# Optimization experiments

Hardware: AMD Instinct MI355X
Metric: run time of the kernel (lower is better)

Reference implementation:

```python
import jax, jax.numpy as jnp
import numpy as np
from jax import lax

DIM, D_STATE, D_CONV, EXPAND = 96, 16, 4, 2
D_INNER = EXPAND * DIM          # 192
DT_RANK = (DIM + 15) // 16      # 6
B_, T_, H_, W_ = 2, 8, 32, 32   # L = T*H*W = 8192 tokens


def setup_inputs() -> dict:
    key = jax.random.key(0)
    ks = jax.random.split(key, 16)
    f = jnp.float32
    rn = lambda k, shape, s=0.02: jax.random.normal(k, shape, dtype=f) * s
    # S4D-real init for A_log, as in mamba_ssm
    A_init = jnp.log(jnp.tile(jnp.arange(1, D_STATE + 1, dtype=f), (D_INNER, 1)))
    return dict(
        x=jax.random.normal(ks[0], (B_, DIM, T_, H_, W_), dtype=f),
        ln_gamma=1.0 + rn(ks[1], (DIM,)),
        ln_beta=rn(ks[2], (DIM,)),
        in_proj_w=rn(ks[3], (2 * D_INNER, DIM)),
        conv_w=rn(ks[4], (D_INNER, 1, D_CONV), 0.1),
        conv_b=rn(ks[5], (D_INNER,)),
        x_proj_w=rn(ks[6], (DT_RANK + 2 * D_STATE, D_INNER)),
        dt_proj_w=rn(ks[7], (D_INNER, DT_RANK), 0.1),
        dt_proj_b=rn(ks[8], (D_INNER,)) + 0.5,
        A_log=A_init,
        D=jnp.ones((D_INNER,), f),
        conv_w_b=rn(ks[9], (D_INNER, 1, D_CONV), 0.1),
        conv_b_b=rn(ks[10], (D_INNER,)),
        x_proj_w_b=rn(ks[11], (DT_RANK + 2 * D_STATE, D_INNER)),
        dt_proj_w_b=rn(ks[12], (D_INNER, DT_RANK), 0.1),
        dt_proj_b_b=rn(ks[13], (D_INNER,)) + 0.5,
        A_log_b=A_init,
        D_b=jnp.ones((D_INNER,), f),
        out_proj_w=rn(ks[14], (DIM, D_INNER)),
    )


def serpentine(x):
    # continues_scan: reverse W on odd H rows so flattened (T,H,W) ordering is a
    # continuous path through the volume. Involutive => also rev_continues_scan.
    return x.at[..., 1::2, :].set(jnp.flip(x[..., 1::2, :], axis=-1))


def layer_norm(x, g, b, eps=1e-5):
    mu = jnp.mean(x, -1, keepdims=True)
    var = jnp.var(x, -1, keepdims=True)
    return (x - mu) * lax.rsqrt(var + eps) * g + b


def mamba_dir(x_in, z, conv_w, conv_b, x_proj_w, dt_proj_w, dt_proj_b, A_log, D):
    # x_in, z: (B, L, d_inner). One directional selective-scan branch.
    xc = lax.conv_general_dilated(
        x_in.swapaxes(1, 2), conv_w, (1,), [(D_CONV - 1, 0)],
        feature_group_count=D_INNER, dimension_numbers=('NCH', 'OIH', 'NCH'))
    xc = jax.nn.silu(xc + conv_b[None, :, None]).swapaxes(1, 2)  # (B,L,d_inner)
    dbl = jnp.einsum('bld,ed->ble', xc, x_proj_w)                # (B,L,dt_rank+2N)
    dt = jax.nn.softplus(
        jnp.einsum('blr,dr->bld', dbl[..., :DT_RANK], dt_proj_w) + dt_proj_b)
    Bm = dbl[..., DT_RANK:DT_RANK + D_STATE]                     # (B,L,N)
    Cm = dbl[..., DT_RANK + D_STATE:]                            # (B,L,N)
    A = -jnp.exp(A_log)                                          # (d_inner,N)

    def step(h, inp):
        dt_t, x_t, B_t, C_t = inp                                # (B,d),(B,d),(B,N),(B,N)
        h = jnp.exp(dt_t[..., None] * A) * h + (dt_t * x_t)[..., None] * B_t[:, None, :]
        return h, jnp.einsum('bdn,bn->bd', h, C_t)

    h0 = jnp.zeros((x_in.shape[0], D_INNER, D_STATE), x_in.dtype)
    xs = (dt.swapaxes(0, 1), xc.swapaxes(0, 1), Bm.swapaxes(0, 1), Cm.swapaxes(0, 1))
    _, ys = lax.scan(step, h0, xs)                               # (L,B,d_inner)
    y = ys.swapaxes(0, 1) + D * xc
    return y * jax.nn.silu(z)


def reference(x, ln_gamma, ln_beta, in_proj_w, conv_w, conv_b, x_proj_w,
              dt_proj_w, dt_proj_b, A_log, D, conv_w_b, conv_b_b, x_proj_w_b,
              dt_proj_w_b, dt_proj_b_b, A_log_b, D_b, out_proj_w):
    B, C, T, H, W = x.shape
    xs = serpentine(x)
    x_flat = xs.reshape(B, C, T * H * W).swapaxes(1, 2)          # (B,L,dim)
    xn = layer_norm(x_flat, ln_gamma, ln_beta)
    xz = jnp.einsum('bld,ed->ble', xn, in_proj_w)                # (B,L,2*d_inner)
    x_in, z = jnp.split(xz, 2, axis=-1)
    y_f = mamba_dir(x_in, z, conv_w, conv_b, x_proj_w, dt_proj_w,
                    dt_proj_b, A_log, D)
    y_b = jnp.flip(
        mamba_dir(jnp.flip(x_in, 1), jnp.flip(z, 1), conv_w_b, conv_b_b,
                  x_proj_w_b, dt_proj_w_b, dt_proj_b_b, A_log_b, D_b), 1)
    out = jnp.einsum('bld,ed->ble', y_f + y_b, out_proj_w)       # (B,L,dim)
    out = out.swapaxes(1, 2).reshape(B, C, T, H, W)
    return serpentine(out)
```

## Files before the change

### kernel.cpp

```cpp
#include <hip/hip_runtime.h>
#include <math.h>

#define LSEQ 8192
#define TS   32
#define NST  8

template<int CTRL>
__device__ __forceinline__ float dpp_add(float x) {
  const int y = __builtin_amdgcn_update_dpp(0, __float_as_int(x), CTRL, 0xF, 0xF, true);
  return x + __int_as_float(y);
}
__device__ __forceinline__ float red8(float x) {
  x = dpp_add<0xB1>(x);
  x = dpp_add<0x4E>(x);
  x += __int_as_float(__builtin_amdgcn_ds_swizzle(__float_as_int(x), 0x101F));
  return x;
}

__global__ __launch_bounds__(256) void k0_wt(const float* __restrict__ xw_f,
    const float* __restrict__ xw_b, const float* __restrict__ in_w,
    const float* __restrict__ ow, float* __restrict__ xwT,
    float* __restrict__ inwT, float* __restrict__ owT) {
  const int step = gridDim.x * 256;
  const int t0 = blockIdx.x * 256 + threadIdx.x;
  for (int idx = t0; idx < 2 * 192 * 40; idx += step) {
    const int dir = idx / (192 * 40), rem = idx - dir * 192 * 40;
    const int k = rem / 40, r = rem - k * 40;
    const float* w = dir ? xw_b : xw_f;
    xwT[idx] = (r < 38) ? w[r * 192 + k] : 0.f;
  }
  for (int idx = t0; idx < 96 * 384; idx += step) {
    const int k = idx / 384, e = idx - k * 384;
    inwT[idx] = in_w[e * 96 + k];
  }
  for (int idx = t0; idx < 192 * 96; idx += step) {
    const int k = idx / 96, e = idx - k * 96;
    owT[idx] = ow[e * 192 + k];
  }
}

__global__ __launch_bounds__(256) void k1_serp_ln(const float* __restrict__ x,
    const float* __restrict__ gam, const float* __restrict__ bet,
    float* __restrict__ xnT) {
  const int b  = blockIdx.x >> 7;
  const int l0 = (blockIdx.x & 127) << 6;
  __shared__ float xs[96][65];
  __shared__ float mu[64], rs[64];
  const int tid = threadIdx.x;
  for (int idx = tid; idx < 96 * 64; idx += 256) {
    const int c = idx >> 6, l = idx & 63;
    const int lg = l0 + l;
    const int hh = (lg >> 5) & 31, w = lg & 31;
    const int lsrc = (hh & 1) ? (lg + 31 - 2 * w) : lg;
    xs[c][l] = x[(b * 96 + c) * LSEQ + lsrc];
  }
  __syncthreads();
  {
    const int l = tid >> 2, k = tid & 3;
    float s = 0.f, s2 = 0.f;
    for (int c = k; c < 96; c += 4) { const float v = xs[c][l]; s += v; s2 += v * v; }
    s  += __shfl_xor(s, 1);  s  += __shfl_xor(s, 2);
    s2 += __shfl_xor(s2, 1); s2 += __shfl_xor(s2, 2);
    if (k == 0) {
      const float m = s * (1.f / 96.f);
      const float var = s2 * (1.f / 96.f) - m * m;
      mu[l] = m; rs[l] = rsqrtf(var + 1e-5f);
    }
  }
  __syncthreads();
  for (int idx = tid; idx < 96 * 64; idx += 256) {
    const int c = idx >> 6, l = idx & 63;
    xnT[c * 16384 + (b << 13) + l0 + l] =
        (xs[c][l] - mu[l]) * rs[l] * gam[c] + bet[c];
  }
}

__global__ __launch_bounds__(256) void k2_inproj(const float* __restrict__ xnT,
    const float* __restrict__ inwT, float* __restrict__ xz) {
  const int m0 = blockIdx.x << 6;
  const int e0 = blockIdx.y << 6;
  __shared__ float As[96][68];
  __shared__ float Ws[96][68];
  const int tid = threadIdx.x;
  for (int idx = tid; idx < 96 * 64; idx += 256) {
    const int k = idx >> 6, r = idx & 63;
    As[k][r] = xnT[(size_t)k * 16384 + m0 + r];
    Ws[k][r] = inwT[k * 384 + e0 + r];
  }
  __syncthreads();
  const int tx = tid & 15, ty = tid >> 4;
  const int la = tx << 2, ea = ty << 2;
  float acc[4][4] = {};
  for (int k = 0; k < 96; ++k) {
    const float4 av = *(const float4*)&As[k][la];
    const float4 bv = *(const float4*)&Ws[k][ea];
    acc[0][0] = fmaf(bv.x, av.x, acc[0][0]); acc[0][1] = fmaf(bv.x, av.y, acc[0][1]);
    acc[0][2] = fmaf(bv.x, av.z, acc[0][2]); acc[0][3] = fmaf(bv.x, av.w, acc[0][3]);
    acc[1][0] = fmaf(bv.y, av.x, acc[1][0]); acc[1][1] = fmaf(bv.y, av.y, acc[1][1]);
    acc[1][2] = fmaf(bv.y, av.z, acc[1][2]); acc[1][3] = fmaf(bv.y, av.w, acc[1][3]);
    acc[2][0] = fmaf(bv.z, av.x, acc[2][0]); acc[2][1] = fmaf(bv.z, av.y, acc[2][1]);
    acc[2][2] = fmaf(bv.z, av.z, acc[2][2]); acc[2][3] = fmaf(bv.z, av.w, acc[2][3]);
    acc[3][0] = fmaf(bv.w, av.x, acc[3][0]); acc[3][1] = fmaf(bv.w, av.y, acc[3][1]);
    acc[3][2] = fmaf(bv.w, av.z, acc[3][2]); acc[3][3] = fmaf(bv.w, av.w, acc[3][3]);
  }
  const int b = m0 >> 13, l0 = m0 & (LSEQ - 1);
  const bool dos = (e0 >= 192);
#pragma unroll
  for (int j = 0; j < 4; ++j) {
    const int e = e0 + ea + j;
    float4 v;
    v.x = acc[j][0]; v.y = acc[j][1]; v.z = acc[j][2]; v.w = acc[j][3];
    if (dos) {
      v.x = v.x / (1.f + __expf(-v.x)); v.y = v.y / (1.f + __expf(-v.y));
      v.z = v.z / (1.f + __expf(-v.z)); v.w = v.w / (1.f + __expf(-v.w));
    }
    *(float4*)(&xz[((size_t)b * 384 + e) * LSEQ + l0 + la]) = v;
  }
}

__global__ __launch_bounds__(256) void k3a_conv(const float* __restrict__ xz,
    const float* __restrict__ cw_f, const float* __restrict__ cb_f,
    const float* __restrict__ cw_b, const float* __restrict__ cb_b,
    float* __restrict__ xc) {
  const int l = (blockIdx.x << 8) + threadIdx.x;
  const int d = blockIdx.y, b = blockIdx.z;
  const float* xin = xz + ((size_t)b * 384 + d) * LSEQ;
  float xv[7];
#pragma unroll
  for (int j = -3; j <= 3; ++j) {
    const int ls = l + j;
    xv[j + 3] = ((unsigned)ls < LSEQ) ? xin[ls] : 0.f;
  }
  float af = cb_f[d], ab = cb_b[d];
#pragma unroll
  for (int j = 0; j < 4; ++j) {
    af = fmaf(cw_f[d * 4 + j], xv[j], af);
    ab = fmaf(cw_b[d * 4 + j], xv[6 - j], ab);
  }
  xc[((size_t)(b)       * 192 + d) * LSEQ + l] = af / (1.f + __expf(-af));
  xc[((size_t)(2 + b)   * 192 + d) * LSEQ + l] = ab / (1.f + __expf(-ab));
}

__global__ __launch_bounds__(256, 2) void k3b_xproj(const float* __restrict__ xc,
    const float* __restrict__ xwT,
    const float* __restrict__ dtw_f, const float* __restrict__ dtb_f,
    const float* __restrict__ dtw_b, const float* __restrict__ dtb_b,
    float* __restrict__ dt, float* __restrict__ Bo, float* __restrict__ Co) {
  __shared__ float xs[96][66];
  __shared__ float part[4][38][65];
  __shared__ float sdbl[6][65];
  const int dirb = blockIdx.y, dir = dirb >> 1;
  const int tid = threadIdx.x;
  const int lane = tid & 63, w = tid >> 6;
  const int l0 = blockIdx.x << 6;
  const float* pcBase = xc + (size_t)dirb * 192 * LSEQ + l0;
  const float* wt = xwT + dir * 192 * 40;
  float acc[38];
#pragma unroll
  for (int r = 0; r < 38; ++r) acc[r] = 0.f;
  const int kb = 24 * w;
  for (int h = 0; h < 2; ++h) {
    __syncthreads();
    for (int idx = tid; idx < 96 * 64; idx += 256) {
      const int kk = idx >> 6, cc = idx & 63;
      xs[kk][cc] = pcBase[(size_t)(96 * h + kk) * LSEQ + cc];
    }
    __syncthreads();
#pragma unroll 4
    for (int kk = 0; kk < 24; ++kk) {
      const int k = 96 * h + kb + kk;
      const float v = xs[kb + kk][lane];
      const float* wk = wt + k * 40;
#pragma unroll
      for (int r = 0; r < 38; ++r) acc[r] = fmaf(wk[r], v, acc[r]);
    }
  }
#pragma unroll
  for (int r = 0; r < 38; ++r) part[w][r][lane] = acc[r];
  __syncthreads();
  {
    const int lq = tid >> 2, g = tid & 3;
    float vB[4], vC[4];
#pragma unroll
    for (int i = 0; i < 4; ++i) {
      const int rB = 6 + 4 * g + i, rC = 22 + 4 * g + i;
      float sB = 0.f, sC = 0.f;
#pragma unroll
      for (int ww = 0; ww < 4; ++ww) {
        sB += part[ww][rB][lq];
        sC += part[ww][rC][lq];
      }
      vB[i] = sB; vC[i] = sC;
    }
    const size_t off = ((size_t)dirb * LSEQ + l0 + lq) * 16 + 4 * g;
    *(float4*)&Bo[off] = make_float4(vB[0], vB[1], vB[2], vB[3]);
    *(float4*)&Co[off] = make_float4(vC[0], vC[1], vC[2], vC[3]);
  }
  for (int r = w; r < 6; r += 4) {
    float s = 0.f;
#pragma unroll
    for (int ww = 0; ww < 4; ++ww) s += part[ww][r][lane];
    sdbl[r][lane] = s;
  }
  __syncthreads();
  const float* dw = dir ? dtw_b : dtw_f;
  const float* db = dir ? dtb_b : dtb_f;
  const float v0 = sdbl[0][lane], v1 = sdbl[1][lane], v2 = sdbl[2][lane],
              v3 = sdbl[3][lane], v4 = sdbl[4][lane], v5 = sdbl[5][lane];
  float* pdt = dt + (size_t)dirb * 192 * LSEQ + l0 + lane;
#pragma unroll 2
  for (int i = 0; i < 48; ++i) {
    const int d = w * 48 + i;
    float s = db[d];
    s = fmaf(dw[d * 6 + 0], v0, s);
    s = fmaf(dw[d * 6 + 1], v1, s);
    s = fmaf(dw[d * 6 + 2], v2, s);
    s = fmaf(dw[d * 6 + 3], v3, s);
    s = fmaf(dw[d * 6 + 4], v4, s);
    s = fmaf(dw[d * 6 + 5], v5, s);
    pdt[(size_t)d * LSEQ] = (s > 20.f) ? s : __logf(1.f + __expf(s));
  }
}

template<int DIR>
__device__ __forceinline__ void scanA_body(
    float2 (*sdt)[32][34], float (*sb)[TS][16],
    const float* __restrict__ dtg, const float* __restrict__ xcg,
    const float* __restrict__ pB, const float* __restrict__ Al,
    float* __restrict__ Pb, float* __restrict__ Hb, int b, int c, int dg) {
  const int tid = threadIdx.x;
  const int dl = tid >> 3, n = tid & 7;
  const int dirb = DIR * 2 + b;
  const int d = (dg << 5) + dl;
  const float Adn1 = -__expf(Al[d * 16 + n]);
  const float Adn2 = -__expf(Al[d * 16 + n + 8]);
  const size_t rowbase = ((size_t)(dirb * 192) + (dg << 5)) * LSEQ;
  const float* dtp = dtg + rowbase;
  const float* xcp = xcg + rowbase;
  const int c0 = c << 8;
  const int sr0 = tid >> 4, spr = (tid & 15) * 2, sr1 = sr0 + 16;
  const int wt = tid >> 2, wf = (tid & 3) * 4;
  {
    const int tc = c0 + (DIR ? (NST - 1) : 0) * TS;
    const float2 a0 = *(const float2*)&dtp[(size_t)sr0 * LSEQ + tc + spr];
    const float2 x0 = *(const float2*)&xcp[(size_t)sr0 * LSEQ + tc + spr];
    const float2 a1 = *(const float2*)&dtp[(size_t)sr1 * LSEQ + tc + spr];
    const float2 x1 = *(const float2*)&xcp[(size_t)sr1 * LSEQ + tc + spr];
    float4 k0; k0.x = a0.x; k0.y = a0.x * x0.x; k0.z = a0.y; k0.w = a0.y * x0.y;
    float4 k1; k1.x = a1.x; k1.y = a1.x * x1.x; k1.z = a1.y; k1.w = a1.y * x1.y;
    *(float4*)&sdt[0][sr0][spr] = k0;
    *(float4*)&sdt[0][sr1][spr] = k1;
    if (tid < 128) {
      const float4 bv = *(const float4*)&pB[(size_t)(tc + wt) * 16 + wf];
      *(float4*)&sb[0][wt][wf] = bv;
    }
  }
  __syncthreads();
  float h1 = 0.f, h2 = 0.f, dts = 0.f;
  int buf = 0;
  for (int i = 0; i < NST; ++i) {
    const int s = DIR ? (NST - 1 - i) : i;
    float2 a0 = make_float2(0.f, 0.f), x0 = a0, a1 = a0, x1 = a0;
    float4 bv = make_float4(0.f, 0.f, 0.f, 0.f);
    if (i + 1 < NST) {
      const int tn = c0 + (DIR ? (s - 1) : (s + 1)) * TS;
      a0 = *(const float2*)&dtp[(size_t)sr0 * LSEQ + tn + spr];
      x0 = *(const float2*)&xcp[(size_t)sr0 * LSEQ + tn + spr];
      a1 = *(const float2*)&dtp[(size_t)sr1 * LSEQ + tn + spr];
      x1 = *(const float2*)&xcp[(size_t)sr1 * LSEQ + tn + spr];
      if (tid < 128) bv = *(const float4*)&pB[(size_t)(tn + wt) * 16 + wf];
    }
#pragma unroll
    for (int tt = 0; tt < TS; ++tt) {
      const int t = DIR ? (TS - 1 - tt) : tt;
      const float2 xv = sdt[buf][dl][t];
      const float B1 = sb[buf][t][n];
      const float B2 = sb[buf][t][n + 8];
      const float e1 = __expf(xv.x * Adn1);
      const float e2 = __expf(xv.x * Adn2);
      h1 = fmaf(e1, h1, xv.y * B1);
      h2 = fmaf(e2, h2, xv.y * B2);
      dts += xv.x;
    }
    if (i + 1 < NST) {
      float4 k0; k0.x = a0.x; k0.y = a0.x * x0.x; k0.z = a0.y; k0.w = a0.y * x0.y;
      float4 k1; k1.x = a1.x; k1.y = a1.x * x1.x; k1.z = a1.y; k1.w = a1.y * x1.y;
      *(float4*)&sdt[buf ^ 1][sr0][spr] = k0;
      *(float4*)&sdt[buf ^ 1][sr1][spr] = k1;
      if (tid < 128) *(float4*)&sb[buf ^ 1][wt][wf] = bv;
    }
    __syncthreads();
    buf ^= 1;
  }
  const int o = ((dirb * 32 + c) * 192 + d) * 16 + n;
  Pb[o]     = __expf(dts * Adn1);
  Pb[o + 8] = __expf(dts * Adn2);
  Hb[o]     = h1;
  Hb[o + 8] = h2;
}

__global__ __launch_bounds__(256) void k4_scanA(const float* __restrict__ dtg,
    const float* __restrict__ xcg, const float* __restrict__ Bo,
    const float* __restrict__ Al_f, const float* __restrict__ Al_b,
    float* __restrict__ Pb, float* __restrict__ Hb) {
  __shared__ float2 sdt[2][32][34];
  __shared__ float sb[2][TS][16];
  const int b = blockIdx.y, c = blockIdx.x & 31, dg = blockIdx.x >> 5;
  const float* pB0 = Bo + (size_t)(0 * 2 + b) * LSEQ * 16;
  const float* pB1 = Bo + (size_t)(1 * 2 + b) * LSEQ * 16;
  if (blockIdx.z == 0) scanA_body<0>(sdt, sb, dtg, xcg, pB0, Al_f, Pb, Hb, b, c, dg);
  else                 scanA_body<1>(sdt, sb, dtg, xcg, pB1, Al_b, Pb, Hb, b, c, dg);
}

__global__ __launch_bounds__(256) void k5_scanB(const float* __restrict__ Pb,
    const float* __restrict__ Hb, float* __restrict__ H0) {
  const int g = blockIdx.x * 256 + threadIdx.x;
  const int dirb = g / 3072, dn = g - dirb * 3072;
  const int dir = dirb >> 1;
  const int base = dirb * (32 * 3072) + dn;
  float h = 0.f;
  if (dir == 0) {
    for (int c = 0; c < 32; ++c) {
      const int o = base + c * 3072;
      H0[o] = h;
      h = fmaf(Pb[o], h, Hb[o]);
    }
  } else {
    for (int c = 31; c >= 0; --c) {
      const int o = base + c * 3072;
      H0[o] = h;
      h = fmaf(Pb[o], h, Hb[o]);
    }
  }
}

template<int DIR>
__device__ __forceinline__ void scanC_body(
    float2 (*sdt)[32][34], float2 (*sbc)[TS][16],
    const float* __restrict__ dtg, const float* __restrict__ xcg,
    const float* __restrict__ pB, const float* __restrict__ pC,
    const float* __restrict__ xz,
    const float* __restrict__ Al, const float* __restrict__ Dv_,
    const float* __restrict__ H0, float* __restrict__ yout,
    int b, int c, int dg) {
  const int tid = threadIdx.x;
  const int dl = tid >> 3, n = tid & 7;
  const int dirb = DIR * 2 + b;
  const int d = (dg << 5) + dl;
  const float Adn1 = -__expf(Al[d * 16 + n]);
  const float Adn2 = -__expf(Al[d * 16 + n + 8]);
  const float Dv = Dv_[d];
  const size_t rowbase = ((size_t)(dirb * 192) + (dg << 5)) * LSEQ;
  const float* dtp = dtg + rowbase;
  const float* xcp = xcg + rowbase;
  const float* xcq = xcg + ((size_t)(dirb * 192) + d) * LSEQ;
  const float* psp = xz + ((size_t)(b * 384) + 192 + d) * LSEQ;
  float* py = yout + ((size_t)(b * 192) + d) * LSEQ;
  const int o = ((dirb * 32 + c) * 192 + d) * 16 + n;
  float h1 = H0[o], h2 = H0[o + 8];
  const int c0 = c << 8;
  const int sr0 = tid >> 4, spr = (tid & 15) * 2, sr1 = sr0 + 16;
  const int sbt = tid >> 3, sbp = (tid & 7) * 2;
  float cx0, cx1, cx2, cx3, sp0, sp1, sp2, sp3;
  {
    const int tc = c0 + (DIR ? (NST - 1) : 0) * TS;
    const float2 a0 = *(const float2*)&dtp[(size_t)sr0 * LSEQ + tc + spr];
    const float2 x0 = *(const float2*)&xcp[(size_t)sr0 * LSEQ + tc + spr];
    const float2 a1 = *(const float2*)&dtp[(size_t)sr1 * LSEQ + tc + spr];
    const float2 x1 = *(const float2*)&xcp[(size_t)sr1 * LSEQ + tc + spr];
    const float2 b2 = *(const float2*)&pB[(size_t)(tc + sbt) * 16 + sbp];
    const float2 c2 = *(const float2*)&pC[(size_t)(tc + sbt) * 16 + sbp];
    float4 k0; k0.x = a0.x; k0.y = a0.x * x0.x; k0.z = a0.y; k0.w = a0.y * x0.y;
    float4 k1; k1.x = a1.x; k1.y = a1.x * x1.x; k1.z = a1.y; k1.w = a1.y * x1.y;
    *(float4*)&sdt[0][sr0][spr] = k0;
    *(float4*)&sdt[0][sr1][spr] = k1;
    *(float4*)&sbc[0][sbt][sbp] = make_float4(b2.x, c2.x, b2.y, c2.y);
    cx0 = xcq[tc + n];      cx1 = xcq[tc + 8 + n];
    cx2 = xcq[tc + 16 + n]; cx3 = xcq[tc + 24 + n];
    sp0 = psp[tc + n];      sp1 = psp[tc + 8 + n];
    sp2 = psp[tc + 16 + n]; sp3 = psp[tc + 24 + n];
  }
  __syncthreads();
  int buf = 0;
  for (int i = 0; i < NST; ++i) {
    const int s = DIR ? (NST - 1 - i) : i;
    const int t0 = c0 + s * TS;
    float2 a0 = make_float2(0.f, 0.f), x0 = a0, a1 = a0, x1 = a0, b2 = a0, c2 = a0;
    float nx0 = 0.f, nx1 = 0.f, nx2 = 0.f, nx3 = 0.f;
    float ns0 = 0.f, ns1 = 0.f, ns2 = 0.f, ns3 = 0.f;
    if (i + 1 < NST) {
      const int tn = c0 + (DIR ? (s - 1) : (s + 1)) * TS;
      a0 = *(const float2*)&dtp[(size_t)sr0 * LSEQ + tn + spr];
      x0 = *(const float2*)&xcp[(size_t)sr0 * LSEQ + tn + spr];
      a1 = *(const float2*)&dtp[(size_t)sr1 * LSEQ + tn + spr];
      x1 = *(const float2*)&xcp[(size_t)sr1 * LSEQ + tn + spr];
      b2 = *(const float2*)&pB[(size_t)(tn + sbt) * 16 + sbp];
      c2 = *(const float2*)&pC[(size_t)(tn + sbt) * 16 + sbp];
      nx0 = xcq[tn + n];      nx1 = xcq[tn + 8 + n];
      nx2 = xcq[tn + 16 + n]; nx3 = xcq[tn + 24 + n];
      ns0 = psp[tn + n];      ns1 = psp[tn + 8 + n];
      ns2 = psp[tn + 16 + n]; ns3 = psp[tn + 24 + n];
    }
    float pq0 = 0.f, pq1 = 0.f, pq2 = 0.f, pq3 = 0.f;
#pragma unroll
    for (int tt = 0; tt < TS; ++tt) {
      const int t = DIR ? (TS - 1 - tt) : tt;
      const float2 xv = sdt[buf][dl][t];
      const float2 v1 = sbc[buf][t][n];
      const float2 v2 = sbc[buf][t][n + 8];
      const float e1 = __expf(xv.x * Adn1);
      const float e2 = __expf(xv.x * Adn2);
      h1 = fmaf(e1, h1, xv.y * v1.x);
      h2 = fmaf(e2, h2, xv.y * v2.x);
      float p = fmaf(h2, v2.y, h1 * v1.y);
      p = red8(p);
      const bool m = ((t & 7) == n);
      if ((t >> 3) == 0)      pq0 = m ? p : pq0;
      else if ((t >> 3) == 1) pq1 = m ? p : pq1;
      else if ((t >> 3) == 2) pq2 = m ? p : pq2;
      else                    pq3 = m ? p : pq3;
    }
    py[t0 + n]      = fmaf(Dv, cx0, pq0) * sp0;
    py[t0 + 8 + n]  = fmaf(Dv, cx1, pq1) * sp1;
    py[t0 + 16 + n] = fmaf(Dv, cx2, pq2) * sp2;
    py[t0 + 24 + n] = fmaf(Dv, cx3, pq3) * sp3;
    if (i + 1 < NST) {
      float4 k0; k0.x = a0.x; k0.y = a0.x * x0.x; k0.z = a0.y; k0.w = a0.y * x0.y;
      float4 k1; k1.x = a1.x; k1.y = a1.x * x1.x; k1.z = a1.y; k1.w = a1.y * x1.y;
      *(float4*)&sdt[buf ^ 1][sr0][spr] = k0;
      *(float4*)&sdt[buf ^ 1][sr1][spr] = k1;
      *(float4*)&sbc[buf ^ 1][sbt][sbp] = make_float4(b2.x, c2.x, b2.y, c2.y);
      cx0 = nx0; cx1 = nx1; cx2 = nx2; cx3 = nx3;
      sp0 = ns0; sp1 = ns1; sp2 = ns2; sp3 = ns3;
    }
    __syncthreads();
    buf ^= 1;
  }
}

__global__ __launch_bounds__(256) void k6_scanC(const float* __restrict__ dtg,
    const float* __restrict__ xcg, const float* __restrict__ Bo,
    const float* __restrict__ Co, const float* __restrict__ xz,
    const float* __restrict__ Al_f, const float* __restrict__ Al_b,
    const float* __restrict__ D_f, const float* __restrict__ D_b,
    const float* __restrict__ H0,
    float* __restrict__ yf, float* __restrict__ yb) {
  __shared__ float2 sdt[2][32][34];
  __shared__ float2 sbc[2][TS][16];
  const int b = blockIdx.y, c = blockIdx.x & 31, dg = blockIdx.x >> 5;
  const float* pB0 = Bo + (size_t)(0 * 2 + b) * LSEQ * 16;
  const float* pB1 = Bo + (size_t)(1 * 2 + b) * LSEQ * 16;
  const float* pC0 = Co + (size_t)(0 * 2 + b) * LSEQ * 16;
  const float* pC1 = Co + (size_t)(1 * 2 + b) * LSEQ * 16;
  if (blockIdx.z == 0)
    scanC_body<0>(sdt, sbc, dtg, xcg, pB0, pC0, xz, Al_f, D_f, H0, yf, b, c, dg);
  else
    scanC_body<1>(sdt, sbc, dtg, xcg, pB1, pC1, xz, Al_b, D_b, H0, yb, b, c, dg);
}

__global__ __launch_bounds__(256) void k7_outproj(const float* __restrict__ yf,
    const float* __restrict__ yb, const float* __restrict__ owT,
    float* __restrict__ out) {
  const int m0 = blockIdx.x << 6;
  const int e0 = blockIdx.y * 48;
  const int b = m0 >> 13, l0 = m0 & (LSEQ - 1);
  __shared__ float As[48][68];
  __shared__ float Ws[48][49];
  const int tid = threadIdx.x;
  const int tx = tid & 15, ty = tid >> 4;
  const int la = tx << 2, ea = ty * 3;
  float acc[3][4] = {};
  for (int kc = 0; kc < 192; kc += 48) {
    for (int idx = tid; idx < 48 * 64; idx += 256) {
      const int k = idx >> 6, l = idx & 63;
      const size_t off = ((size_t)b * 192 + kc + k) * LSEQ + l0 + l;
      As[k][l] = yf[off] + yb[off];
    }
    for (int idx = tid; idx < 48 * 48; idx += 256) {
      const int k = idx / 48, e = idx - k * 48;
      Ws[k][e] = owT[(kc + k) * 96 + e0 + e];
    }
    __syncthreads();
#pragma unroll 4
    for (int k = 0; k < 48; ++k) {
      const float4 a4 = *(const float4*)&As[k][la];
      const float w0 = Ws[k][ea], w1 = Ws[k][ea + 1], w2 = Ws[k][ea + 2];
      acc[0][0] = fmaf(w0, a4.x, acc[0][0]); acc[0][1] = fmaf(w0, a4.y, acc[0][1]);
      acc[0][2] = fmaf(w0, a4.z, acc[0][2]); acc[0][3] = fmaf(w0, a4.w, acc[0][3]);
      acc[1][0] = fmaf(w1, a4.x, acc[1][0]); acc[1][1] = fmaf(w1, a4.y, acc[1][1]);
      acc[1][2] = fmaf(w1, a4.z, acc[1][2]); acc[1][3] = fmaf(w1, a4.w, acc[1][3]);
      acc[2][0] = fmaf(w2, a4.x, acc[2][0]); acc[2][1] = fmaf(w2, a4.y, acc[2][1]);
      acc[2][2] = fmaf(w2, a4.z, acc[2][2]); acc[2][3] = fmaf(w2, a4.w, acc[2][3]);
    }
    __syncthreads();
  }
#pragma unroll
  for (int j = 0; j < 3; ++j) {
    const int e = e0 + ea + j;
#pragma unroll
    for (int i = 0; i < 4; ++i) {
      const int l = l0 + la + i;
      const int hh = (l >> 5) & 31, ww = l & 31;
      const int lp = (hh & 1) ? (l + 31 - 2 * ww) : l;
      out[((size_t)b * 96 + e) * LSEQ + lp] = acc[j][i];
    }
  }
}

extern "C" void kernel_launch(void* const* d_in, const int* in_sizes, int n_in,
                              void* d_out, int out_size, void* d_ws, size_t ws_size,
                              hipStream_t stream) {
  const float* x     = (const float*)d_in[0];
  const float* ln_g  = (const float*)d_in[1];
  const float* ln_b  = (const float*)d_in[2];
  const float* in_w  = (const float*)d_in[3];
  const float* cw_f  = (const float*)d_in[4];
  const float* cb_f  = (const float*)d_in[5];
  const float* xw_f  = (const float*)d_in[6];
  const float* dtw_f = (const float*)d_in[7];
  const float* dtb_f = (const float*)d_in[8];
  const float* Al_f  = (const float*)d_in[9];
  const float* D_f   = (const float*)d_in[10];
  const float* cw_b  = (const float*)d_in[11];
  const float* cb_b  = (const float*)d_in[12];
  const float* xw_b  = (const float*)d_in[13];
  const float* dtw_b = (const float*)d_in[14];
  const float* dtb_b = (const float*)d_in[15];
  const float* Al_b  = (const float*)d_in[16];
  const float* D_b   = (const float*)d_in[17];
  const float* ow    = (const float*)d_in[18];
  float* out = (float*)d_out;

  float* ws = (float*)d_ws;
  float* xnT  = ws; ws += (size_t)16384 * 96;
  float* xz   = ws; ws += (size_t)2 * 384 * LSEQ;
  float* xc   = ws; ws += (size_t)4 * 192 * LSEQ;
  float* dt   = ws; ws += (size_t)4 * 192 * LSEQ;
  float* Bo   = ws; ws += (size_t)4 * LSEQ * 16;
  float* Co   = ws; ws += (size_t)4 * LSEQ * 16;
  float* yf   = ws; ws += (size_t)2 * 192 * LSEQ;
  float* yb   = ws; ws += (size_t)2 * 192 * LSEQ;
  float* Pb   = ws; ws += (size_t)4 * 32 * 192 * 16;
  float* Hb   = ws; ws += (size_t)4 * 32 * 192 * 16;
  float* H0   = ws; ws += (size_t)4 * 32 * 192 * 16;
  float* xwT  = ws; ws += (size_t)2 * 192 * 40;
  float* inwT = ws; ws += (size_t)96 * 384;
  float* owT  = ws; ws += (size_t)192 * 96;

  k0_wt<<<dim3(64), dim3(256), 0, stream>>>(xw_f, xw_b, in_w, ow, xwT, inwT, owT);
  k1_serp_ln<<<dim3(256), dim3(256), 0, stream>>>(x, ln_g, ln_b, xnT);
  k2_inproj<<<dim3(256, 6), dim3(256), 0, stream>>>(xnT, inwT, xz);
  k3a_conv<<<dim3(32, 192, 2), dim3(256), 0, stream>>>(xz, cw_f, cb_f, cw_b, cb_b, xc);
  k3b_xproj<<<dim3(128, 4), dim3(256), 0, stream>>>(xc, xwT,
      dtw_f, dtb_f, dtw_b, dtb_b, dt, Bo, Co);
  k4_scanA<<<dim3(192, 2, 2), dim3(256), 0, stream>>>(dt, xc, Bo,
      Al_f, Al_b, Pb, Hb);
  k5_scanB<<<dim3(48), dim3(256), 0, stream>>>(Pb, Hb, H0);
  k6_scanC<<<dim3(192, 2, 2), dim3(256), 0, stream>>>(dt, xc, Bo, Co,
      xz, Al_f, Al_b, D_f, D_b, H0, yf, yb);
  k7_outproj<<<dim3(256, 2), dim3(256), 0, stream>>>(yf, yb, owT, out);
}
```

Before: 197.1 us.

## Rewrite x_proj as register-tiled shared-memory GEMM and stage dt weights in LDS

The x_proj kernel moves from a per-lane 38-row accumulator with a K-split across waves and a cross-wave reduction to a 2D register-tiled GEMM. Each thread computes a 3x4 output tile, with activations and padded weights (48 columns) staged in shared memory in 48-wide K chunks. This removes the large accumulator array and the partial-sum reduction, and replaces scalar global weight loads with LDS reads. dt_proj weights are also cached in LDS. The cost is more synchronisation per K chunk and some wasted work on the padded rows.

```diff
diff --git a/kernel.cpp b/kernel.cpp
--- a/kernel.cpp
+++ b/kernel.cpp
@@ -23,9 +23,9 @@
     float* __restrict__ inwT, float* __restrict__ owT) {
   const int step = gridDim.x * 256;
   const int t0 = blockIdx.x * 256 + threadIdx.x;
-  for (int idx = t0; idx < 2 * 192 * 40; idx += step) {
-    const int dir = idx / (192 * 40), rem = idx - dir * 192 * 40;
-    const int k = rem / 40, r = rem - k * 40;
+  for (int idx = t0; idx < 2 * 192 * 48; idx += step) {
+    const int dir = idx / (192 * 48), rem = idx - dir * 192 * 48;
+    const int k = rem / 48, r = rem - k * 48;
     const float* w = dir ? xw_b : xw_f;
     xwT[idx] = (r < 38) ? w[r * 192 + k] : 0.f;
   }
@@ -146,78 +146,80 @@
     const float* __restrict__ dtw_f, const float* __restrict__ dtb_f,
     const float* __restrict__ dtw_b, const float* __restrict__ dtb_b,
     float* __restrict__ dt, float* __restrict__ Bo, float* __restrict__ Co) {
-  __shared__ float xs[96][66];
-  __shared__ float part[4][38][65];
-  __shared__ float sdbl[6][65];
+  __shared__ float As[48][68];
+  __shared__ float Wc[48][48];
+  __shared__ float outs[40][68];
+  __shared__ float dtwl[1152];
   const int dirb = blockIdx.y, dir = dirb >> 1;
   const int tid = threadIdx.x;
   const int lane = tid & 63, w = tid >> 6;
   const int l0 = blockIdx.x << 6;
   const float* pcBase = xc + (size_t)dirb * 192 * LSEQ + l0;
-  const float* wt = xwT + dir * 192 * 40;
-  float acc[38];
-#pragma unroll
-  for (int r = 0; r < 38; ++r) acc[r] = 0.f;
-  const int kb = 24 * w;
-  for (int h = 0; h < 2; ++h) {
-    __syncthreads();
-    for (int idx = tid; idx < 96 * 64; idx += 256) {
-      const int kk = idx >> 6, cc = idx & 63;
-      xs[kk][cc] = pcBase[(size_t)(96 * h + kk) * LSEQ + cc];
+  const float* wt = xwT + dir * 192 * 48;
+  const float* dtwp = dir ? dtw_b : dtw_f;
+  for (int idx = tid; idx < 1152; idx += 256) dtwl[idx] = dtwp[idx];
+  const int tx = tid & 15, ty = tid >> 4;
+  const int la = tx << 2, ra = ty * 3;
+  float acc[3][4] = {};
+  for (int kc = 0; kc < 192; kc += 48) {
+    if (kc) __syncthreads();
+    for (int idx = tid; idx < 48 * 64; idx += 256) {
+      const int k = idx >> 6, cc = idx & 63;
+      As[k][cc] = pcBase[(size_t)(kc + k) * LSEQ + cc];
+    }
+    for (int idx = tid; idx < 48 * 48; idx += 256) {
+      const int k = idx / 48, r = idx - k * 48;
+      Wc[k][r] = wt[(kc + k) * 48 + r];
     }
     __syncthreads();
 #pragma unroll 4
-    for (int kk = 0; kk < 24; ++kk) {
-      const int k = 96 * h + kb + kk;
-      const float v = xs[kb + kk][lane];
-      const float* wk = wt + k * 40;
-#pragma unroll
-      for (int r = 0; r < 38; ++r) acc[r] = fmaf(wk[r], v, acc[r]);
-    }
-  }
-#pragma unroll
-  for (int r = 0; r < 38; ++r) part[w][r][lane] = acc[r];
+    for (int k = 0; k < 48; ++k) {
+      const float4 a4 = *(const float4*)&As[k][la];
+      const float w0 = Wc[k][ra], w1 = Wc[k][ra + 1], w2 = Wc[k][ra + 2];
+      acc[0][0] = fmaf(w0, a4.x, acc[0][0]); acc[0][1] = fmaf(w0, a4.y, acc[0][1]);
+      acc[0][2] = fmaf(w0, a4.z, acc[0][2]); acc[0][3] = fmaf(w0, a4.w, acc[0][3]);
+      acc[1][0] = fmaf(w1, a4.x, acc[1][0]); acc[1][1] = fmaf(w1, a4.y, acc[1][1]);
+      acc[1][2] = fmaf(w1, a4.z, acc[1][2]); acc[1][3] = fmaf(w1, a4.w, acc[1][3]);
+      acc[2][0] = fmaf(w2, a4.x, acc[2][0]); acc[2][1] = fmaf(w2, a4.y, acc[2][1]);
+      acc[2][2] = fmaf(w2, a4.z, acc[2][2]); acc[2][3] = fmaf(w2, a4.w, acc[2][3]);
+    }
+  }
+  __syncthreads();
+#pragma unroll
+  for (int j = 0; j < 3; ++j) {
+    const int r = ra + j;
+    if (r < 40) {
+#pragma unroll
+      for (int i = 0; i < 4; ++i) outs[r][la + i] = acc[j][i];
+    }
+  }
   __syncthreads();
   {
     const int lq = tid >> 2, g = tid & 3;
     float vB[4], vC[4];
 #pragma unroll
     for (int i = 0; i < 4; ++i) {
-      const int rB = 6 + 4 * g + i, rC = 22 + 4 * g + i;
-      float sB = 0.f, sC = 0.f;
-#pragma unroll
-      for (int ww = 0; ww < 4; ++ww) {
-        sB += part[ww][rB][lq];
-        sC += part[ww][rC][lq];
-      }
-      vB[i] = sB; vC[i] = sC;
+      vB[i] = outs[6 + 4 * g + i][lq];
+      vC[i] = outs[22 + 4 * g + i][lq];
     }
     const size_t off = ((size_t)dirb * LSEQ + l0 + lq) * 16 + 4 * g;
     *(float4*)&Bo[off] = make_float4(vB[0], vB[1], vB[2], vB[3]);
     *(float4*)&Co[off] = make_float4(vC[0], vC[1], vC[2], vC[3]);
   }
-  for (int r = w; r < 6; r += 4) {
-    float s = 0.f;
-#pragma unroll
-    for (int ww = 0; ww < 4; ++ww) s += part[ww][r][lane];
-    sdbl[r][lane] = s;
-  }
-  __syncthreads();
-  const float* dw = dir ? dtw_b : dtw_f;
   const float* db = dir ? dtb_b : dtb_f;
-  const float v0 = sdbl[0][lane], v1 = sdbl[1][lane], v2 = sdbl[2][lane],
-              v3 = sdbl[3][lane], v4 = sdbl[4][lane], v5 = sdbl[5][lane];
+  const float v0 = outs[0][lane], v1 = outs[1][lane], v2 = outs[2][lane],
+              v3 = outs[3][lane], v4 = outs[4][lane], v5 = outs[5][lane];
   float* pdt = dt + (size_t)dirb * 192 * LSEQ + l0 + lane;
 #pragma unroll 2
   for (int i = 0; i < 48; ++i) {
     const int d = w * 48 + i;
     float s = db[d];
-    s = fmaf(dw[d * 6 + 0], v0, s);
-    s = fmaf(dw[d * 6 + 1], v1, s);
-    s = fmaf(dw[d * 6 + 2], v2, s);
-    s = fmaf(dw[d * 6 + 3], v3, s);
-    s = fmaf(dw[d * 6 + 4], v4, s);
-    s = fmaf(dw[d * 6 + 5], v5, s);
+    s = fmaf(dtwl[d * 6 + 0], v0, s);
+    s = fmaf(dtwl[d * 6 + 1], v1, s);
+    s = fmaf(dtwl[d * 6 + 2], v2, s);
+    s = fmaf(dtwl[d * 6 + 3], v3, s);
+    s = fmaf(dtwl[d * 6 + 4], v4, s);
+    s = fmaf(dtwl[d * 6 + 5], v5, s);
     pdt[(size_t)d * LSEQ] = (s > 20.f) ? s : __logf(1.f + __expf(s));
   }
 }
@@ -543,7 +545,7 @@
   float* Pb   = ws; ws += (size_t)4 * 32 * 192 * 16;
   float* Hb   = ws; ws += (size_t)4 * 32 * 192 * 16;
   float* H0   = ws; ws += (size_t)4 * 32 * 192 * 16;
-  float* xwT  = ws; ws += (size_t)2 * 192 * 40;
+  float* xwT  = ws; ws += (size_t)2 * 192 * 48;
   float* inwT = ws; ws += (size_t)96 * 384;
   float* owT  = ws; ws += (size_t)192 * 96;
 
```

Result: faster. 189.8 us (median of 2 runs) (-3.7%).
